# Kernel optimization log

Measured on AMD Instinct MI355X. Metric: run time of the kernel, lower is better.

The kernel has to match this reference:

```python
import jax, jax.numpy as jnp
import numpy as np

HEADS = 20
HEAD_DIM = 64  # 1280 / 20
IP_SCALE = 1.0


def _split_heads(x, B):
    # [B, S, H*D] -> [B, H, S, D]
    return x.reshape(B, -1, HEADS, HEAD_DIM).transpose(0, 2, 1, 3)


def _merge_heads(x, B):
    # [B, H, S, D] -> [B, S, H*D]
    return x.transpose(0, 2, 1, 3).reshape(B, -1, HEADS * HEAD_DIM)


def _sdpa(q, k, v):
    # q:[B,H,Sq,D] k,v:[B,H,Sk,D]
    scale = 1.0 / jnp.sqrt(jnp.asarray(HEAD_DIM, q.dtype))
    scores = jnp.einsum('bhqd,bhkd->bhqk', q, k) * scale
    probs = jax.nn.softmax(scores, axis=-1)
    return jnp.einsum('bhqk,bhkd->bhqd', probs, v)


def setup_inputs() -> dict:
    key = jax.random.key(0)
    ks = jax.random.split(key, 10)
    B, S, D = 8, 4096, 1280
    Ctx, Cdim = 77, 2048
    Adim = 768
    inp = {
        'hidden_states': jax.random.normal(ks[0], (B, S, D), jnp.float32),
        'encoder_hidden_states': jax.random.normal(ks[1], (B, Ctx, Cdim), jnp.float32),
        'adapter_embeds': jax.random.normal(ks[2], (B, 1, Adim), jnp.float32),
        'Wq': jax.random.normal(ks[3], (D, D), jnp.float32) * 0.02,
        'Wk': jax.random.normal(ks[4], (Cdim, D), jnp.float32) * 0.02,
        'Wv': jax.random.normal(ks[5], (Cdim, D), jnp.float32) * 0.02,
        'Wk_adapter': jax.random.normal(ks[6], (Adim, D), jnp.float32) * 0.02,
        'Wv_adapter': jax.random.normal(ks[7], (Adim, D), jnp.float32) * 0.02,
        'Wo': jax.random.normal(ks[8], (D, D), jnp.float32) * 0.02,
        'bo': jnp.zeros((D,), jnp.float32),
    }
    return inp


def reference(hidden_states, encoder_hidden_states, adapter_embeds,
              Wq, Wk, Wv, Wk_adapter, Wv_adapter, Wo, bo):
    B = hidden_states.shape[0]

    # base cross-attention projections
    q = _split_heads(hidden_states @ Wq, B)                 # [B,H,S,D]
    k = _split_heads(encoder_hidden_states @ Wk, B)         # [B,H,77,D]
    v = _split_heads(encoder_hidden_states @ Wv, B)
    out = _merge_heads(_sdpa(q, k, v), B)                   # [B,S,H*D]

    # IP-adapter branch: single-token K/V, shares the same query
    k_ip = _split_heads(adapter_embeds @ Wk_adapter, B)     # [B,H,1,D]
    v_ip = _split_heads(adapter_embeds @ Wv_adapter, B)
    out_ip = _merge_heads(_sdpa(q, k_ip, v_ip), B)

    merged = out + IP_SCALE * out_ip
    return merged @ Wo + bo
```

## Files before the change

### kernel.cpp

```cpp
#include <hip/hip_runtime.h>
#include <hip/hip_bf16.h>
#include <cstdint>
#include <cstddef>

typedef __hip_bfloat16 bf16_t;
typedef __attribute__((ext_vector_type(8))) __bf16 bf16x8;
typedef __attribute__((ext_vector_type(4))) float f32x4;

__device__ __forceinline__ void gld_lds16(const void* g, void* l) {
    __builtin_amdgcn_global_load_lds(
        (const __attribute__((address_space(1))) void*)(g),
        (__attribute__((address_space(3))) void*)(l), 16, 0, 0);
}

__global__ void k_cast(const float* __restrict__ in, bf16_t* __restrict__ out, long n) {
    long i = ((long)blockIdx.x * blockDim.x + threadIdx.x) * 4;
    if (i >= n) return;
    float4 v = *(const float4*)(in + i);
    out[i + 0] = __float2bfloat16(v.x);
    out[i + 1] = __float2bfloat16(v.y);
    out[i + 2] = __float2bfloat16(v.z);
    out[i + 3] = __float2bfloat16(v.w);
}

__global__ void k_cast_pad(const float* __restrict__ in, bf16_t* __restrict__ out,
                           int rows_in, int rows_out, int cols) {
    long i = ((long)blockIdx.x * blockDim.x + threadIdx.x) * 4;
    long n = (long)rows_out * cols;
    if (i >= n) return;
    int r = (int)(i / cols);
    if (r < rows_in) {
        float4 v = *(const float4*)(in + i);
        out[i + 0] = __float2bfloat16(v.x);
        out[i + 1] = __float2bfloat16(v.y);
        out[i + 2] = __float2bfloat16(v.z);
        out[i + 3] = __float2bfloat16(v.w);
    } else {
        bf16_t z = __float2bfloat16(0.f);
        out[i + 0] = z; out[i + 1] = z; out[i + 2] = z; out[i + 3] = z;
    }
}

__global__ void k_transpose_cast2(const float* __restrict__ in0, bf16_t* __restrict__ out0,
                                  const float* __restrict__ in1, bf16_t* __restrict__ out1,
                                  int R, int C) {
    __shared__ float tile[32][33];
    const float* in = blockIdx.z ? in1 : in0;
    bf16_t* out = blockIdx.z ? out1 : out0;
    int bx = blockIdx.x * 32;
    int by = blockIdx.y * 32;
    int tx = threadIdx.x & 31, ty = threadIdx.x >> 5;
    #pragma unroll
    for (int j = 0; j < 32; j += 8)
        tile[ty + j][tx] = in[(size_t)(by + ty + j) * C + bx + tx];
    __syncthreads();
    #pragma unroll
    for (int j = 0; j < 32; j += 8)
        out[(size_t)(bx + ty + j) * R + by + tx] = __float2bfloat16(tile[tx][ty + j]);
}

__global__ void k_adapter(const float* __restrict__ ae, const float* __restrict__ Wva,
                          float* __restrict__ vip) {
    int g = blockIdx.x * 256 + threadIdx.x;
    int b = g / 1280, n = g % 1280;
    const float* a = ae + b * 768;
    float acc = 0.f;
    for (int k = 0; k < 768; ++k) acc += a[k] * Wva[(size_t)k * 1280 + n];
    vip[g] = acc;
}

template <bool OUT_BF16, bool ADD_BIAS, bool SWZ>
__global__ __launch_bounds__(256, 2) void k_gemm_bt(
    const bf16_t* __restrict__ A, const bf16_t* __restrict__ Bt,
    void* __restrict__ Cv, const float* __restrict__ bias, int M, int N, int K,
    int snt, int mtx) {
    __shared__ __align__(16) bf16_t As[128 * 32];
    __shared__ __align__(16) bf16_t Bs[128 * 32];
    const int tid = threadIdx.x;
    int m0, n0;
    if constexpr (SWZ) {
        int id = blockIdx.x;
        int xcd = id & 7, j = id >> 3;
        m0 = (xcd * mtx + j / snt) * 128;
        n0 = (j % snt) * 128;
    } else {
        m0 = blockIdx.y * 128;
        n0 = blockIdx.x * 128;
    }
    const int wave = tid >> 6, lane = tid & 63;
    const int wm = (wave >> 1) * 64, wn = (wave & 1) * 64;
    const int quad = lane >> 4, l16 = lane & 15;

    f32x4 acc[4][4] = {};

    const int c0 = tid, c1 = tid + 256;
    const int r0 = c0 >> 2, o0 = (c0 & 3) * 8;
    const int r1 = c1 >> 2, o1 = (c1 & 3) * 8;
    const bf16_t* a0 = A + (size_t)(m0 + r0) * K + o0;
    const bf16_t* a1 = A + (size_t)(m0 + r1) * K + o1;
    const bf16_t* b0 = Bt + (size_t)(n0 + r0) * K + o0;
    const bf16_t* b1 = Bt + (size_t)(n0 + r1) * K + o1;

    for (int k0 = 0; k0 < K; k0 += 32) {
        __syncthreads();
        gld_lds16(a0 + k0, As + c0 * 8);
        gld_lds16(a1 + k0, As + c1 * 8);
        gld_lds16(b0 + k0, Bs + c0 * 8);
        gld_lds16(b1 + k0, Bs + c1 * 8);
        __syncthreads();
        bf16x8 af[4], bfv[4];
        #pragma unroll
        for (int t = 0; t < 4; ++t) {
            af[t]  = *(const bf16x8*)(As + (wm + t * 16 + l16) * 32 + quad * 8);
            bfv[t] = *(const bf16x8*)(Bs + (wn + t * 16 + l16) * 32 + quad * 8);
        }
        #pragma unroll
        for (int mt = 0; mt < 4; ++mt)
            #pragma unroll
            for (int nt = 0; nt < 4; ++nt)
                acc[mt][nt] = __builtin_amdgcn_mfma_f32_16x16x32_bf16(af[mt], bfv[nt], acc[mt][nt], 0, 0, 0);
    }

    if constexpr (OUT_BF16) {
        bf16_t* C = (bf16_t*)Cv;
        #pragma unroll
        for (int mt = 0; mt < 4; ++mt)
            #pragma unroll
            for (int rg = 0; rg < 4; ++rg) {
                int row = m0 + wm + mt * 16 + quad * 4 + rg;
                #pragma unroll
                for (int nt = 0; nt < 4; ++nt) {
                    int col = n0 + wn + nt * 16 + l16;
                    C[(size_t)row * N + col] = __float2bfloat16(acc[mt][nt][rg]);
                }
            }
    } else {
        float* C = (float*)Cv;
        float bv[4];
        #pragma unroll
        for (int nt = 0; nt < 4; ++nt)
            bv[nt] = ADD_BIAS ? bias[n0 + wn + nt * 16 + l16] : 0.f;
        #pragma unroll
        for (int mt = 0; mt < 4; ++mt)
            #pragma unroll
            for (int rg = 0; rg < 4; ++rg) {
                int row = m0 + wm + mt * 16 + quad * 4 + rg;
                #pragma unroll
                for (int nt = 0; nt < 4; ++nt) {
                    int col = n0 + wn + nt * 16 + l16;
                    C[(size_t)row * N + col] = acc[mt][nt][rg] + bv[nt];
                }
            }
    }
}

template <bool OUT_BF16, bool ADD_BIAS, int KC>
__global__ __launch_bounds__(512, 2) void k_gemm256(
    const bf16_t* __restrict__ A, const bf16_t* __restrict__ Bt,
    void* __restrict__ Cv, const float* __restrict__ bias,
    int N, int snt, int mtx) {
    __shared__ __align__(16) bf16_t As[2][256 * 64];
    __shared__ __align__(16) bf16_t Bs[2][256 * 64];
    const int tid = threadIdx.x;
    const int id = blockIdx.x;
    const int xcd = id & 7, jb = id >> 3;
    const int m0 = (xcd * mtx + jb / snt) * 256;
    const int n0 = (jb % snt) * 256;
    const int wave = tid >> 6, lane = tid & 63;
    const int wm = wave >> 2, wn = wave & 3;
    const int quad = lane >> 4, l16 = lane & 15;

    const int lr0 = tid >> 3;
    const int cst = ((tid & 7) * 8) ^ ((lr0 & 7) * 8);
    const bf16_t* pA0 = A + (size_t)(m0 + lr0) * KC + cst;
    const bf16_t* pA1 = pA0 + (size_t)128 * KC;
    const bf16_t* pB0 = Bt + (size_t)(n0 + ((lr0 >> 5) << 6) + (lr0 & 31)) * KC + cst;
    const bf16_t* pB1 = pB0 + (size_t)128 * KC;
    const int eA0 = tid * 8, eA1 = 4096 + tid * 8;

    const int xorc = (l16 & 7) * 8;
    const int c0x = (quad * 8) ^ xorc;
    const int c1x = (32 + quad * 8) ^ xorc;
    const int arow = (wm * 64 + l16) * 64;
    const int brow = (wn * 32 + l16) * 64;

    f32x4 acc[8][4] = {};
    bf16x8 afA[4][2], afB[4][2], bf0[2][2], bf1[2][2];

#define SA0_(WB, T) do { size_t ko_ = (size_t)(T) * 64; \
    gld_lds16(pA0 + ko_, &As[WB][eA0]); gld_lds16(pA1 + ko_, &As[WB][eA1]); } while (0)
#define SA1_(WB, T) do { size_t ko_ = (size_t)(T) * 64 + (size_t)64 * KC; \
    gld_lds16(pA0 + ko_, &As[WB][8192 + eA0]); gld_lds16(pA1 + ko_, &As[WB][8192 + eA1]); } while (0)
#define SB0_(WB, T) do { size_t ko_ = (size_t)(T) * 64; \
    gld_lds16(pB0 + ko_, &Bs[WB][eA0]); gld_lds16(pB1 + ko_, &Bs[WB][eA1]); } while (0)
#define SB1_(WB, T) do { size_t ko_ = (size_t)(T) * 64 + (size_t)32 * KC; \
    gld_lds16(pB0 + ko_, &Bs[WB][8192 + eA0]); gld_lds16(pB1 + ko_, &Bs[WB][8192 + eA1]); } while (0)
#define RD_AFA(RB_) do { _Pragma("unroll") for (int mt = 0; mt < 4; ++mt) { \
    const bf16_t* p_ = &As[RB_][arow + mt * 1024]; \
    afA[mt][0] = *(const bf16x8*)(p_ + c0x); afA[mt][1] = *(const bf16x8*)(p_ + c1x); } } while (0)
#define RD_AFB(RB_) do { _Pragma("unroll") for (int mt = 0; mt < 4; ++mt) { \
    const bf16_t* p_ = &As[RB_][8192 + arow + mt * 1024]; \
    afB[mt][0] = *(const bf16x8*)(p_ + c0x); afB[mt][1] = *(const bf16x8*)(p_ + c1x); } } while (0)
#define RD_BF0(RB_) do { _Pragma("unroll") for (int nt = 0; nt < 2; ++nt) { \
    const bf16_t* p_ = &Bs[RB_][brow + nt * 1024]; \
    bf0[nt][0] = *(const bf16x8*)(p_ + c0x); bf0[nt][1] = *(const bf16x8*)(p_ + c1x); } } while (0)
#define RD_BF1(RB_) do { _Pragma("unroll") for (int nt = 0; nt < 2; ++nt) { \
    const bf16_t* p_ = &Bs[RB_][8192 + brow + nt * 1024]; \
    bf1[nt][0] = *(const bf16x8*)(p_ + c0x); bf1[nt][1] = *(const bf16x8*)(p_ + c1x); } } while (0)
#define MMA_(AF, BF, MB, NB) do { _Pragma("unroll") \
    for (int mt = 0; mt < 4; ++mt) _Pragma("unroll") \
    for (int nt = 0; nt < 2; ++nt) _Pragma("unroll") \
    for (int ks = 0; ks < 2; ++ks) \
      acc[(MB) + mt][(NB) + nt] = __builtin_amdgcn_mfma_f32_16x16x32_bf16( \
          AF[mt][ks], BF[nt][ks], acc[(MB) + mt][(NB) + nt], 0, 0, 0); } while (0)
#define BAR_ asm volatile("s_barrier" ::: "memory")
#define VM_(n) asm volatile("s_waitcnt vmcnt(" #n ")" ::: "memory")
#define LG_(n) do { asm volatile("s_waitcnt lgkmcnt(" #n ")" ::: "memory"); \
    __builtin_amdgcn_sched_barrier(0); } while (0)
#define P1_ __builtin_amdgcn_s_setprio(1)
#define P0_ __builtin_amdgcn_s_setprio(0)

#define TILE_(T, RB) do { \
    RD_BF1(RB); SA1_((RB) ^ 1, (T) + 1); VM_(8); BAR_; \
    LG_(4); P1_; MMA_(afA, bf0, 0, 0); P0_; BAR_; \
    RD_AFB(RB); SA0_(RB, (T) + 2); VM_(8); BAR_; \
    LG_(8); P1_; MMA_(afA, bf1, 0, 2); P0_; BAR_; \
    RD_AFA((RB) ^ 1); SB0_(RB, (T) + 2); VM_(8); BAR_; \
    LG_(8); P1_; MMA_(afB, bf0, 4, 0); P0_; BAR_; \
    RD_BF0((RB) ^ 1); SB1_(RB, (T) + 2); VM_(8); BAR_; \
    P1_; MMA_(afB, bf1, 4, 2); P0_; BAR_; \
  } while (0)

    const int NT = KC >> 6;

    SA0_(0, 0); SB0_(0, 0); SB1_(0, 0); SA1_(0, 0);
    SA0_(1, 1); SB0_(1, 1); SB1_(1, 1);
    VM_(8);
    BAR_;
    RD_AFA(0); RD_BF0(0);

    #pragma unroll 1
    for (int t = 0; t < NT - 2; t += 2) {
        TILE_(t, 0);
        TILE_(t + 1, 1);
    }

    RD_BF1(0); SA1_(1, NT - 1); VM_(8); BAR_;
    LG_(4); P1_; MMA_(afA, bf0, 0, 0); P0_; BAR_;
    RD_AFB(0); VM_(6); BAR_;
    LG_(8); P1_; MMA_(afA, bf1, 0, 2); P0_; BAR_;
    RD_AFA(1); VM_(4); BAR_;
    LG_(8); P1_; MMA_(afB, bf0, 4, 0); P0_; BAR_;
    RD_BF0(1); VM_(2); BAR_;
    P1_; MMA_(afB, bf1, 4, 2); P0_; BAR_;
    RD_BF1(1); VM_(0); BAR_;
    RD_AFB(1);
    LG_(12); P1_; MMA_(afA, bf0, 0, 0); P0_;
    LG_(8);  P1_; MMA_(afA, bf1, 0, 2); P0_;
    LG_(0);  P1_; MMA_(afB, bf0, 4, 0); P0_;
    P1_; MMA_(afB, bf1, 4, 2); P0_;

#undef SA0_
#undef SA1_
#undef SB0_
#undef SB1_
#undef RD_AFA
#undef RD_AFB
#undef RD_BF0
#undef RD_BF1
#undef MMA_
#undef BAR_
#undef VM_
#undef LG_
#undef P1_
#undef P0_
#undef TILE_

    if constexpr (OUT_BF16) {
        bf16_t* C = (bf16_t*)Cv;
        __syncthreads();
        bf16_t* eb = wm ? (bf16_t*)Bs : (bf16_t*)As;
        #pragma unroll
        for (int mt = 0; mt < 8; ++mt)
            #pragma unroll
            for (int rg = 0; rg < 4; ++rg) {
                int rr = (mt >> 2) * 64 + (mt & 3) * 16 + quad * 4 + rg;
                #pragma unroll
                for (int nt = 0; nt < 4; ++nt)
                    eb[rr * 256 + wn * 64 + nt * 16 + l16] = __float2bfloat16(acc[mt][nt][rg]);
            }
        __syncthreads();
        #pragma unroll
        for (int pass = 0; pass < 16; ++pass) {
            const bf16_t* sb = (pass < 8) ? (const bf16_t*)As : (const bf16_t*)Bs;
            int r = pass * 16 + (tid >> 5);
            int cc = (tid & 31) * 8;
            *(int4*)(&C[(size_t)(m0 + r) * N + n0 + cc]) =
                *(const int4*)(sb + (r & 127) * 256 + cc);
        }
    } else {
        float* C = (float*)Cv;
        float bv[4];
        #pragma unroll
        for (int nt = 0; nt < 4; ++nt)
            bv[nt] = ADD_BIAS ? bias[n0 + wn * 64 + nt * 16 + l16] : 0.f;
        #pragma unroll
        for (int mt = 0; mt < 8; ++mt)
            #pragma unroll
            for (int rg = 0; rg < 4; ++rg) {
                int row = m0 + wm * 128 + (mt >> 2) * 64 + (mt & 3) * 16 + quad * 4 + rg;
                #pragma unroll
                for (int nt = 0; nt < 4; ++nt) {
                    int col = n0 + wn * 64 + nt * 16 + l16;
                    C[(size_t)row * N + col] = acc[mt][nt][rg] + bv[nt];
                }
            }
    }
}

__global__ __launch_bounds__(256, 2) void k_attn(
    const bf16_t* __restrict__ Q, const bf16_t* __restrict__ KV,
    const float* __restrict__ vip, bf16_t* __restrict__ Mrg) {
    __shared__ __align__(16) bf16_t Qs[128 * 64];
    __shared__ __align__(16) bf16_t Ks[96 * 64];
    __shared__ __align__(16) bf16_t Vt[64 * 96];
    __shared__ __align__(16) bf16_t Ps[128 * 96];
    const int tid = threadIdx.x;
    const int qb = blockIdx.x, h = blockIdx.y, b = blockIdx.z;
    const int wave = tid >> 6, lane = tid & 63;
    const int quad = lane >> 4, l16 = lane & 15;

    const bf16_t* Qg = Q + ((size_t)(b * 4096 + qb * 128)) * 1280 + h * 64;
    #pragma unroll
    for (int j = 0; j < 4; ++j) {
        int c = tid + j * 256;
        int r = c >> 3, o = (c & 7) * 8;
        gld_lds16(Qg + (size_t)r * 1280 + o, Qs + c * 8);
    }
    bf16_t z = __float2bfloat16(0.f);
    for (int i = 77 * 64 + tid; i < 96 * 64; i += 256) Ks[i] = z;
    for (int i = tid; i < 64 * 19; i += 256) {
        int d = i / 19, kk = 77 + i % 19;
        Vt[d * 96 + kk] = z;
    }
    for (int c = tid; c < 616; c += 256) {
        int r = c >> 3, o = (c & 7) * 8;
        size_t gi = ((size_t)(b * 77 + r)) * 2560 + h * 64 + o;
        int4 kv = *(const int4*)(KV + gi);
        *(int4*)(Ks + r * 64 + o) = kv;
        int4 vv = *(const int4*)(KV + gi + 1280);
        const bf16_t* ve = (const bf16_t*)&vv;
        #pragma unroll
        for (int j = 0; j < 8; ++j) Vt[(o + j) * 96 + r] = ve[j];
    }
    __syncthreads();

    f32x4 sacc[2][6] = {};
    #pragma unroll
    for (int ks = 0; ks < 2; ++ks) {
        bf16x8 aq[2], bk[6];
        #pragma unroll
        for (int mt = 0; mt < 2; ++mt)
            aq[mt] = *(const bf16x8*)(Qs + (wave * 32 + mt * 16 + l16) * 64 + ks * 32 + quad * 8);
        #pragma unroll
        for (int nt = 0; nt < 6; ++nt)
            bk[nt] = *(const bf16x8*)(Ks + (nt * 16 + l16) * 64 + ks * 32 + quad * 8);
        #pragma unroll
        for (int mt = 0; mt < 2; ++mt)
            #pragma unroll
            for (int nt = 0; nt < 6; ++nt)
                sacc[mt][nt] = __builtin_amdgcn_mfma_f32_16x16x32_bf16(aq[mt], bk[nt], sacc[mt][nt], 0, 0, 0);
    }
    #pragma unroll
    for (int mt = 0; mt < 2; ++mt)
        #pragma unroll
        for (int nt = 0; nt < 6; ++nt)
            #pragma unroll
            for (int rg = 0; rg < 4; ++rg) {
                int row = wave * 32 + mt * 16 + quad * 4 + rg;
                int col = nt * 16 + l16;
                Ps[row * 96 + col] = __float2bfloat16(sacc[mt][nt][rg] * 0.125f);
            }
    __syncthreads();

    {
        int row = tid >> 1, half = tid & 1;
        int cbeg = half ? 39 : 0, cend = half ? 77 : 39;
        bf16_t* prow = Ps + row * 96;
        float mx = -1e30f;
        for (int c = cbeg; c < cend; ++c) mx = fmaxf(mx, __bfloat162float(prow[c]));
        mx = fmaxf(mx, __shfl_xor(mx, 1));
        float sm = 0.f;
        for (int c = cbeg; c < cend; ++c) sm += __expf(__bfloat162float(prow[c]) - mx);
        sm += __shfl_xor(sm, 1);
        float inv = 1.f / sm;
        for (int c = cbeg; c < cend; ++c)
            prow[c] = __float2bfloat16(__expf(__bfloat162float(prow[c]) - mx) * inv);
    }
    __syncthreads();

    f32x4 oacc[2][4] = {};
    #pragma unroll
    for (int ks = 0; ks < 3; ++ks) {
        bf16x8 ap[2], bv[4];
        #pragma unroll
        for (int mt = 0; mt < 2; ++mt)
            ap[mt] = *(const bf16x8*)(Ps + (wave * 32 + mt * 16 + l16) * 96 + ks * 32 + quad * 8);
        #pragma unroll
        for (int nt = 0; nt < 4; ++nt)
            bv[nt] = *(const bf16x8*)(Vt + (nt * 16 + l16) * 96 + ks * 32 + quad * 8);
        #pragma unroll
        for (int mt = 0; mt < 2; ++mt)
            #pragma unroll
            for (int nt = 0; nt < 4; ++nt)
                oacc[mt][nt] = __builtin_amdgcn_mfma_f32_16x16x32_bf16(ap[mt], bv[nt], oacc[mt][nt], 0, 0, 0);
    }
    __syncthreads();
    #pragma unroll
    for (int nt = 0; nt < 4; ++nt) {
        int col = nt * 16 + l16;
        float add = vip[b * 1280 + h * 64 + col];
        #pragma unroll
        for (int mt = 0; mt < 2; ++mt)
            #pragma unroll
            for (int rg = 0; rg < 4; ++rg) {
                int row = wave * 32 + mt * 16 + quad * 4 + rg;
                Ps[row * 64 + col] = __float2bfloat16(oacc[mt][nt][rg] + add);
            }
    }
    __syncthreads();
    #pragma unroll
    for (int pass = 0; pass < 4; ++pass) {
        int r = pass * 32 + (tid >> 3);
        int cc = (tid & 7) * 8;
        *(int4*)(Mrg + ((size_t)(b * 4096 + qb * 128 + r)) * 1280 + h * 64 + cc) =
            *(const int4*)(Ps + r * 64 + cc);
    }
}

extern "C" void kernel_launch(void* const* d_in, const int* in_sizes, int n_in,
                              void* d_out, int out_size, void* d_ws, size_t ws_size,
                              hipStream_t stream) {
    (void)in_sizes; (void)n_in; (void)out_size; (void)ws_size;
    const float* hs  = (const float*)d_in[0];
    const float* enc = (const float*)d_in[1];
    const float* ae  = (const float*)d_in[2];
    const float* Wq  = (const float*)d_in[3];
    const float* Wk  = (const float*)d_in[4];
    const float* Wv  = (const float*)d_in[5];
    const float* Wva = (const float*)d_in[7];
    const float* Wo  = (const float*)d_in[8];
    const float* bo  = (const float*)d_in[9];
    float* out = (float*)d_out;

    char* ws = (char*)d_ws;
    size_t off = 0;
    auto alloc = [&](size_t bytes) -> void* {
        void* p = ws + off;
        off += (bytes + 255) & ~(size_t)255;
        return p;
    };
    bf16_t* Xb   = (bf16_t*)alloc((size_t)32768 * 1280 * 2);
    bf16_t* Qb   = (bf16_t*)alloc((size_t)32768 * 1280 * 2);
    bf16_t* Mrg  = (bf16_t*)alloc((size_t)32768 * 1280 * 2);
    bf16_t* Eb   = (bf16_t*)alloc((size_t)640 * 2048 * 2);
    bf16_t* WqT  = (bf16_t*)alloc((size_t)1280 * 1280 * 2);
    bf16_t* WkvT = (bf16_t*)alloc((size_t)2560 * 2048 * 2);
    bf16_t* WoT  = (bf16_t*)alloc((size_t)1280 * 1280 * 2);
    bf16_t* KVc  = (bf16_t*)alloc((size_t)640 * 2560 * 2);
    float*  vip  = (float*)alloc((size_t)8 * 1280 * 4);

    k_cast<<<40960, 256, 0, stream>>>(hs, Xb, (long)32768 * 1280);
    k_cast_pad<<<1280, 256, 0, stream>>>(enc, Eb, 616, 640, 2048);
    k_transpose_cast2<<<dim3(40, 40, 2), 256, 0, stream>>>(Wq, WqT, Wo, WoT, 1280, 1280);
    k_transpose_cast2<<<dim3(40, 64, 2), 256, 0, stream>>>(Wk, WkvT, Wv, WkvT + (size_t)1280 * 2048, 2048, 1280);
    k_adapter<<<40, 256, 0, stream>>>(ae, Wva, vip);

    k_gemm256<true, false, 1280><<<640, 512, 0, stream>>>(Xb, WqT, Qb, nullptr, 1280, 5, 16);
    k_gemm_bt<true, false, false><<<dim3(20, 5), 256, 0, stream>>>(Eb, WkvT, KVc, nullptr, 640, 2560, 2048, 0, 0);

    k_attn<<<dim3(32, 20, 8), 256, 0, stream>>>(Qb, KVc, vip, Mrg);

    k_gemm256<false, true, 1280><<<640, 512, 0, stream>>>(Mrg, WoT, out, bo, 1280, 5, 16);
}
```

Measured before the change: 830.8 us.

## Merge prolog kernels, fold KV GEMM into Q GEMM launch, register-resident softmax

Fuses the hidden-state and encoder casts into one launch and the four weight transposes into another. It folds the small encoder K/V projection into the large Q-projection GEMM grid as extra blocks, with K now a runtime value. The GEMM main loop's waitcnt/barrier schedule changes, and attention softmax now runs on MFMA accumulators in registers with shuffles instead of a shared-memory pass. The LDS strides for P and V are padded to avoid bank conflicts. This cuts launch count and a shared-memory round trip, but runtime K may cost some loop codegen quality and the retuned wait counts risk subtle hazards.

```diff
diff --git a/kernel.cpp b/kernel.cpp
--- a/kernel.cpp
+++ b/kernel.cpp
@@ -13,40 +13,43 @@
         (__attribute__((address_space(3))) void*)(l), 16, 0, 0);
 }
 
-__global__ void k_cast(const float* __restrict__ in, bf16_t* __restrict__ out, long n) {
-    long i = ((long)blockIdx.x * blockDim.x + threadIdx.x) * 4;
-    if (i >= n) return;
-    float4 v = *(const float4*)(in + i);
-    out[i + 0] = __float2bfloat16(v.x);
-    out[i + 1] = __float2bfloat16(v.y);
-    out[i + 2] = __float2bfloat16(v.z);
-    out[i + 3] = __float2bfloat16(v.w);
-}
-
-__global__ void k_cast_pad(const float* __restrict__ in, bf16_t* __restrict__ out,
-                           int rows_in, int rows_out, int cols) {
-    long i = ((long)blockIdx.x * blockDim.x + threadIdx.x) * 4;
-    long n = (long)rows_out * cols;
-    if (i >= n) return;
-    int r = (int)(i / cols);
-    if (r < rows_in) {
-        float4 v = *(const float4*)(in + i);
-        out[i + 0] = __float2bfloat16(v.x);
-        out[i + 1] = __float2bfloat16(v.y);
-        out[i + 2] = __float2bfloat16(v.z);
-        out[i + 3] = __float2bfloat16(v.w);
+__global__ void k_prolog(const float* __restrict__ hs, bf16_t* __restrict__ Xb,
+                         const float* __restrict__ enc, bf16_t* __restrict__ Eb) {
+    if (blockIdx.x < 40960) {
+        long i = ((long)blockIdx.x * 256 + threadIdx.x) * 4;
+        float4 v = *(const float4*)(hs + i);
+        Xb[i + 0] = __float2bfloat16(v.x);
+        Xb[i + 1] = __float2bfloat16(v.y);
+        Xb[i + 2] = __float2bfloat16(v.z);
+        Xb[i + 3] = __float2bfloat16(v.w);
     } else {
-        bf16_t z = __float2bfloat16(0.f);
-        out[i + 0] = z; out[i + 1] = z; out[i + 2] = z; out[i + 3] = z;
-    }
-}
-
-__global__ void k_transpose_cast2(const float* __restrict__ in0, bf16_t* __restrict__ out0,
-                                  const float* __restrict__ in1, bf16_t* __restrict__ out1,
-                                  int R, int C) {
+        long i = ((long)(blockIdx.x - 40960) * 256 + threadIdx.x) * 4;
+        int r = (int)(i / 2048);
+        if (r < 616) {
+            float4 v = *(const float4*)(enc + i);
+            Eb[i + 0] = __float2bfloat16(v.x);
+            Eb[i + 1] = __float2bfloat16(v.y);
+            Eb[i + 2] = __float2bfloat16(v.z);
+            Eb[i + 3] = __float2bfloat16(v.w);
+        } else {
+            bf16_t z = __float2bfloat16(0.f);
+            Eb[i + 0] = z; Eb[i + 1] = z; Eb[i + 2] = z; Eb[i + 3] = z;
+        }
+    }
+}
+
+__global__ void k_transpose_cast4(const float* __restrict__ Wq, bf16_t* __restrict__ WqT,
+                                  const float* __restrict__ Wo, bf16_t* __restrict__ WoT,
+                                  const float* __restrict__ Wk, const float* __restrict__ Wv,
+                                  bf16_t* __restrict__ WkvT) {
     __shared__ float tile[32][33];
-    const float* in = blockIdx.z ? in1 : in0;
-    bf16_t* out = blockIdx.z ? out1 : out0;
+    int z = blockIdx.z;
+    if (z < 2 && blockIdx.y >= 40) return;
+    const float* in; bf16_t* out; int R, C;
+    if (z == 0)      { in = Wq; out = WqT; R = 1280; C = 1280; }
+    else if (z == 1) { in = Wo; out = WoT; R = 1280; C = 1280; }
+    else if (z == 2) { in = Wk; out = WkvT; R = 2048; C = 1280; }
+    else             { in = Wv; out = WkvT + (size_t)1280 * 2048; R = 2048; C = 1280; }
     int bx = blockIdx.x * 32;
     int by = blockIdx.y * 32;
     int tx = threadIdx.x & 31, ty = threadIdx.x >> 5;
@@ -69,113 +72,40 @@
     vip[g] = acc;
 }
 
-template <bool OUT_BF16, bool ADD_BIAS, bool SWZ>
-__global__ __launch_bounds__(256, 2) void k_gemm_bt(
-    const bf16_t* __restrict__ A, const bf16_t* __restrict__ Bt,
-    void* __restrict__ Cv, const float* __restrict__ bias, int M, int N, int K,
-    int snt, int mtx) {
-    __shared__ __align__(16) bf16_t As[128 * 32];
-    __shared__ __align__(16) bf16_t Bs[128 * 32];
-    const int tid = threadIdx.x;
-    int m0, n0;
-    if constexpr (SWZ) {
-        int id = blockIdx.x;
-        int xcd = id & 7, j = id >> 3;
-        m0 = (xcd * mtx + j / snt) * 128;
-        n0 = (j % snt) * 128;
-    } else {
-        m0 = blockIdx.y * 128;
-        n0 = blockIdx.x * 128;
-    }
-    const int wave = tid >> 6, lane = tid & 63;
-    const int wm = (wave >> 1) * 64, wn = (wave & 1) * 64;
-    const int quad = lane >> 4, l16 = lane & 15;
-
-    f32x4 acc[4][4] = {};
-
-    const int c0 = tid, c1 = tid + 256;
-    const int r0 = c0 >> 2, o0 = (c0 & 3) * 8;
-    const int r1 = c1 >> 2, o1 = (c1 & 3) * 8;
-    const bf16_t* a0 = A + (size_t)(m0 + r0) * K + o0;
-    const bf16_t* a1 = A + (size_t)(m0 + r1) * K + o1;
-    const bf16_t* b0 = Bt + (size_t)(n0 + r0) * K + o0;
-    const bf16_t* b1 = Bt + (size_t)(n0 + r1) * K + o1;
-
-    for (int k0 = 0; k0 < K; k0 += 32) {
-        __syncthreads();
-        gld_lds16(a0 + k0, As + c0 * 8);
-        gld_lds16(a1 + k0, As + c1 * 8);
-        gld_lds16(b0 + k0, Bs + c0 * 8);
-        gld_lds16(b1 + k0, Bs + c1 * 8);
-        __syncthreads();
-        bf16x8 af[4], bfv[4];
-        #pragma unroll
-        for (int t = 0; t < 4; ++t) {
-            af[t]  = *(const bf16x8*)(As + (wm + t * 16 + l16) * 32 + quad * 8);
-            bfv[t] = *(const bf16x8*)(Bs + (wn + t * 16 + l16) * 32 + quad * 8);
-        }
-        #pragma unroll
-        for (int mt = 0; mt < 4; ++mt)
-            #pragma unroll
-            for (int nt = 0; nt < 4; ++nt)
-                acc[mt][nt] = __builtin_amdgcn_mfma_f32_16x16x32_bf16(af[mt], bfv[nt], acc[mt][nt], 0, 0, 0);
-    }
-
-    if constexpr (OUT_BF16) {
-        bf16_t* C = (bf16_t*)Cv;
-        #pragma unroll
-        for (int mt = 0; mt < 4; ++mt)
-            #pragma unroll
-            for (int rg = 0; rg < 4; ++rg) {
-                int row = m0 + wm + mt * 16 + quad * 4 + rg;
-                #pragma unroll
-                for (int nt = 0; nt < 4; ++nt) {
-                    int col = n0 + wn + nt * 16 + l16;
-                    C[(size_t)row * N + col] = __float2bfloat16(acc[mt][nt][rg]);
-                }
-            }
-    } else {
-        float* C = (float*)Cv;
-        float bv[4];
-        #pragma unroll
-        for (int nt = 0; nt < 4; ++nt)
-            bv[nt] = ADD_BIAS ? bias[n0 + wn + nt * 16 + l16] : 0.f;
-        #pragma unroll
-        for (int mt = 0; mt < 4; ++mt)
-            #pragma unroll
-            for (int rg = 0; rg < 4; ++rg) {
-                int row = m0 + wm + mt * 16 + quad * 4 + rg;
-                #pragma unroll
-                for (int nt = 0; nt < 4; ++nt) {
-                    int col = n0 + wn + nt * 16 + l16;
-                    C[(size_t)row * N + col] = acc[mt][nt][rg] + bv[nt];
-                }
-            }
-    }
-}
-
-template <bool OUT_BF16, bool ADD_BIAS, int KC>
+template <bool OUT_BF16, bool ADD_BIAS>
 __global__ __launch_bounds__(512, 2) void k_gemm256(
     const bf16_t* __restrict__ A, const bf16_t* __restrict__ Bt,
     void* __restrict__ Cv, const float* __restrict__ bias,
-    int N, int snt, int mtx) {
+    int N, int K, int snt, int mtx, int nq,
+    const bf16_t* __restrict__ A2, const bf16_t* __restrict__ Bt2,
+    bf16_t* __restrict__ C2, int N2, int K2, int snt2) {
     __shared__ __align__(16) bf16_t As[2][256 * 64];
     __shared__ __align__(16) bf16_t Bs[2][256 * 64];
     const int tid = threadIdx.x;
     const int id = blockIdx.x;
-    const int xcd = id & 7, jb = id >> 3;
-    const int m0 = (xcd * mtx + jb / snt) * 256;
-    const int n0 = (jb % snt) * 256;
+    const bf16_t* Ain; const bf16_t* Btin; void* Cout;
+    int Nn, Kd, m0, n0;
+    if (id < nq) {
+        int xcd = id & 7, j = id >> 3;
+        m0 = (xcd * mtx + j / snt) * 256;
+        n0 = (j % snt) * 256;
+        Ain = A; Btin = Bt; Cout = Cv; Nn = N; Kd = K;
+    } else {
+        int j = id - nq;
+        m0 = (j / snt2) * 256;
+        n0 = (j % snt2) * 256;
+        Ain = A2; Btin = Bt2; Cout = (void*)C2; Nn = N2; Kd = K2;
+    }
     const int wave = tid >> 6, lane = tid & 63;
     const int wm = wave >> 2, wn = wave & 3;
     const int quad = lane >> 4, l16 = lane & 15;
 
     const int lr0 = tid >> 3;
     const int cst = ((tid & 7) * 8) ^ ((lr0 & 7) * 8);
-    const bf16_t* pA0 = A + (size_t)(m0 + lr0) * KC + cst;
-    const bf16_t* pA1 = pA0 + (size_t)128 * KC;
-    const bf16_t* pB0 = Bt + (size_t)(n0 + ((lr0 >> 5) << 6) + (lr0 & 31)) * KC + cst;
-    const bf16_t* pB1 = pB0 + (size_t)128 * KC;
+    const bf16_t* pA0 = Ain + (size_t)(m0 + lr0) * Kd + cst;
+    const bf16_t* pA1 = pA0 + (size_t)128 * Kd;
+    const bf16_t* pB0 = Btin + (size_t)(n0 + ((lr0 >> 5) << 6) + (lr0 & 31)) * Kd + cst;
+    const bf16_t* pB1 = pB0 + (size_t)128 * Kd;
     const int eA0 = tid * 8, eA1 = 4096 + tid * 8;
 
     const int xorc = (l16 & 7) * 8;
@@ -189,11 +119,11 @@
 
 #define SA0_(WB, T) do { size_t ko_ = (size_t)(T) * 64; \
     gld_lds16(pA0 + ko_, &As[WB][eA0]); gld_lds16(pA1 + ko_, &As[WB][eA1]); } while (0)
-#define SA1_(WB, T) do { size_t ko_ = (size_t)(T) * 64 + (size_t)64 * KC; \
+#define SA1_(WB, T) do { size_t ko_ = (size_t)(T) * 64 + (size_t)64 * Kd; \
     gld_lds16(pA0 + ko_, &As[WB][8192 + eA0]); gld_lds16(pA1 + ko_, &As[WB][8192 + eA1]); } while (0)
 #define SB0_(WB, T) do { size_t ko_ = (size_t)(T) * 64; \
     gld_lds16(pB0 + ko_, &Bs[WB][eA0]); gld_lds16(pB1 + ko_, &Bs[WB][eA1]); } while (0)
-#define SB1_(WB, T) do { size_t ko_ = (size_t)(T) * 64 + (size_t)32 * KC; \
+#define SB1_(WB, T) do { size_t ko_ = (size_t)(T) * 64 + (size_t)32 * Kd; \
     gld_lds16(pB0 + ko_, &Bs[WB][8192 + eA0]); gld_lds16(pB1 + ko_, &Bs[WB][8192 + eA1]); } while (0)
 #define RD_AFA(RB_) do { _Pragma("unroll") for (int mt = 0; mt < 4; ++mt) { \
     const bf16_t* p_ = &As[RB_][arow + mt * 1024]; \
@@ -220,38 +150,46 @@
 #define P1_ __builtin_amdgcn_s_setprio(1)
 #define P0_ __builtin_amdgcn_s_setprio(0)
 
-#define TILE_(T, RB) do { \
-    RD_BF1(RB); SA1_((RB) ^ 1, (T) + 1); VM_(8); BAR_; \
-    LG_(4); P1_; MMA_(afA, bf0, 0, 0); P0_; BAR_; \
-    RD_AFB(RB); SA0_(RB, (T) + 2); VM_(8); BAR_; \
-    LG_(8); P1_; MMA_(afA, bf1, 0, 2); P0_; BAR_; \
-    RD_AFA((RB) ^ 1); SB0_(RB, (T) + 2); VM_(8); BAR_; \
-    LG_(8); P1_; MMA_(afB, bf0, 4, 0); P0_; BAR_; \
-    RD_BF0((RB) ^ 1); SB1_(RB, (T) + 2); VM_(8); BAR_; \
+#define TILEFULL(T, RB) do { \
+    RD_BF1(RB); SA1_((RB) ^ 1, (T) + 1); \
+    asm volatile("s_waitcnt lgkmcnt(8)" ::: "memory"); \
+    BAR_; LG_(0); \
+    P1_; MMA_(afA, bf0, 0, 0); P0_; BAR_; \
+    RD_AFB(RB); SA0_(RB, (T) + 2); \
+    BAR_; LG_(0); \
+    P1_; MMA_(afA, bf1, 0, 2); P0_; BAR_; \
+    RD_AFA((RB) ^ 1); SB0_(RB, (T) + 2); \
+    BAR_; LG_(0); \
+    P1_; MMA_(afB, bf0, 4, 0); P0_; BAR_; \
+    RD_BF0((RB) ^ 1); SB1_(RB, (T) + 2); \
+    VM_(6); \
+    BAR_; LG_(0); \
     P1_; MMA_(afB, bf1, 4, 2); P0_; BAR_; \
   } while (0)
 
-    const int NT = KC >> 6;
+    const int NT = Kd >> 6;
 
     SA0_(0, 0); SB0_(0, 0); SB1_(0, 0); SA1_(0, 0);
     SA0_(1, 1); SB0_(1, 1); SB1_(1, 1);
-    VM_(8);
+    VM_(6);
     BAR_;
     RD_AFA(0); RD_BF0(0);
 
     #pragma unroll 1
     for (int t = 0; t < NT - 2; t += 2) {
-        TILE_(t, 0);
-        TILE_(t + 1, 1);
-    }
-
-    RD_BF1(0); SA1_(1, NT - 1); VM_(8); BAR_;
-    LG_(4); P1_; MMA_(afA, bf0, 0, 0); P0_; BAR_;
-    RD_AFB(0); VM_(6); BAR_;
-    LG_(8); P1_; MMA_(afA, bf1, 0, 2); P0_; BAR_;
-    RD_AFA(1); VM_(4); BAR_;
-    LG_(8); P1_; MMA_(afB, bf0, 4, 0); P0_; BAR_;
-    RD_BF0(1); VM_(2); BAR_;
+        TILEFULL(t, 0);
+        TILEFULL(t + 1, 1);
+    }
+
+    RD_BF1(0); SA1_(1, NT - 1);
+    asm volatile("s_waitcnt lgkmcnt(8)" ::: "memory");
+    BAR_; LG_(0);
+    P1_; MMA_(afA, bf0, 0, 0); P0_; BAR_;
+    RD_AFB(0); VM_(6); BAR_; LG_(0);
+    P1_; MMA_(afA, bf1, 0, 2); P0_; BAR_;
+    RD_AFA(1); VM_(4); BAR_; LG_(0);
+    P1_; MMA_(afB, bf0, 4, 0); P0_; BAR_;
+    RD_BF0(1); VM_(2); BAR_; LG_(0);
     P1_; MMA_(afB, bf1, 4, 2); P0_; BAR_;
     RD_BF1(1); VM_(0); BAR_;
     RD_AFB(1);
@@ -274,10 +212,10 @@
 #undef LG_
 #undef P1_
 #undef P0_
-#undef TILE_
+#undef TILEFULL
 
     if constexpr (OUT_BF16) {
-        bf16_t* C = (bf16_t*)Cv;
+        bf16_t* C = (bf16_t*)Cout;
         __syncthreads();
         bf16_t* eb = wm ? (bf16_t*)Bs : (bf16_t*)As;
         #pragma unroll
@@ -295,11 +233,11 @@
             const bf16_t* sb = (pass < 8) ? (const bf16_t*)As : (const bf16_t*)Bs;
             int r = pass * 16 + (tid >> 5);
             int cc = (tid & 31) * 8;
-            *(int4*)(&C[(size_t)(m0 + r) * N + n0 + cc]) =
+            *(int4*)(&C[(size_t)(m0 + r) * Nn + n0 + cc]) =
                 *(const int4*)(sb + (r & 127) * 256 + cc);
         }
     } else {
-        float* C = (float*)Cv;
+        float* C = (float*)Cout;
         float bv[4];
         #pragma unroll
         for (int nt = 0; nt < 4; ++nt)
@@ -312,7 +250,7 @@
                 #pragma unroll
                 for (int nt = 0; nt < 4; ++nt) {
                     int col = n0 + wn * 64 + nt * 16 + l16;
-                    C[(size_t)row * N + col] = acc[mt][nt][rg] + bv[nt];
+                    C[(size_t)row * Nn + col] = acc[mt][nt][rg] + bv[nt];
                 }
             }
     }
@@ -321,10 +259,11 @@
 __global__ __launch_bounds__(256, 2) void k_attn(
     const bf16_t* __restrict__ Q, const bf16_t* __restrict__ KV,
     const float* __restrict__ vip, bf16_t* __restrict__ Mrg) {
+    constexpr int PST = 104, VST = 104;
     __shared__ __align__(16) bf16_t Qs[128 * 64];
     __shared__ __align__(16) bf16_t Ks[96 * 64];
-    __shared__ __align__(16) bf16_t Vt[64 * 96];
-    __shared__ __align__(16) bf16_t Ps[128 * 96];
+    __shared__ __align__(16) bf16_t Vt[64 * VST];
+    __shared__ __align__(16) bf16_t Ps[128 * PST];
     const int tid = threadIdx.x;
     const int qb = blockIdx.x, h = blockIdx.y, b = blockIdx.z;
     const int wave = tid >> 6, lane = tid & 63;
@@ -341,7 +280,7 @@
     for (int i = 77 * 64 + tid; i < 96 * 64; i += 256) Ks[i] = z;
     for (int i = tid; i < 64 * 19; i += 256) {
         int d = i / 19, kk = 77 + i % 19;
-        Vt[d * 96 + kk] = z;
+        Vt[d * VST + kk] = z;
     }
     for (int c = tid; c < 616; c += 256) {
         int r = c >> 3, o = (c & 7) * 8;
@@ -351,7 +290,7 @@
         int4 vv = *(const int4*)(KV + gi + 1280);
         const bf16_t* ve = (const bf16_t*)&vv;
         #pragma unroll
-        for (int j = 0; j < 8; ++j) Vt[(o + j) * 96 + r] = ve[j];
+        for (int j = 0; j < 8; ++j) Vt[(o + j) * VST + r] = ve[j];
     }
     __syncthreads();
 
@@ -371,31 +310,40 @@
             for (int nt = 0; nt < 6; ++nt)
                 sacc[mt][nt] = __builtin_amdgcn_mfma_f32_16x16x32_bf16(aq[mt], bk[nt], sacc[mt][nt], 0, 0, 0);
     }
-    #pragma unroll
-    for (int mt = 0; mt < 2; ++mt)
-        #pragma unroll
-        for (int nt = 0; nt < 6; ++nt)
-            #pragma unroll
-            for (int rg = 0; rg < 4; ++rg) {
-                int row = wave * 32 + mt * 16 + quad * 4 + rg;
+
+    #pragma unroll
+    for (int mt = 0; mt < 2; ++mt) {
+        #pragma unroll
+        for (int rg = 0; rg < 4; ++rg) {
+            float v[6];
+            float mx = -1e30f;
+            #pragma unroll
+            for (int nt = 0; nt < 6; ++nt) {
                 int col = nt * 16 + l16;
-                Ps[row * 96 + col] = __float2bfloat16(sacc[mt][nt][rg] * 0.125f);
+                v[nt] = sacc[mt][nt][rg] * 0.125f;
+                if (col < 77) mx = fmaxf(mx, v[nt]);
             }
-    __syncthreads();
-
-    {
-        int row = tid >> 1, half = tid & 1;
-        int cbeg = half ? 39 : 0, cend = half ? 77 : 39;
-        bf16_t* prow = Ps + row * 96;
-        float mx = -1e30f;
-        for (int c = cbeg; c < cend; ++c) mx = fmaxf(mx, __bfloat162float(prow[c]));
-        mx = fmaxf(mx, __shfl_xor(mx, 1));
-        float sm = 0.f;
-        for (int c = cbeg; c < cend; ++c) sm += __expf(__bfloat162float(prow[c]) - mx);
-        sm += __shfl_xor(sm, 1);
-        float inv = 1.f / sm;
-        for (int c = cbeg; c < cend; ++c)
-            prow[c] = __float2bfloat16(__expf(__bfloat162float(prow[c]) - mx) * inv);
+            mx = fmaxf(mx, __shfl_xor(mx, 1));
+            mx = fmaxf(mx, __shfl_xor(mx, 2));
+            mx = fmaxf(mx, __shfl_xor(mx, 4));
+            mx = fmaxf(mx, __shfl_xor(mx, 8));
+            float sm = 0.f;
+            #pragma unroll
+            for (int nt = 0; nt < 6; ++nt) {
+                int col = nt * 16 + l16;
+                v[nt] = (col < 77) ? __expf(v[nt] - mx) : 0.f;
+                sm += v[nt];
+            }
+            sm += __shfl_xor(sm, 1);
+            sm += __shfl_xor(sm, 2);
+            sm += __shfl_xor(sm, 4);
+            sm += __shfl_xor(sm, 8);
+            float inv = 1.f / sm;
+            int row = wave * 32 + mt * 16 + quad * 4 + rg;
+            #pragma unroll
+            for (int nt = 0; nt < 6; ++nt)
+                Ps[row * PST + nt * 16 + l16] = __float2bfloat16(v[nt] * inv);
+        }
     }
     __syncthreads();
 
@@ -405,10 +353,10 @@
         bf16x8 ap[2], bv[4];
         #pragma unroll
         for (int mt = 0; mt < 2; ++mt)
-            ap[mt] = *(const bf16x8*)(Ps + (wave * 32 + mt * 16 + l16) * 96 + ks * 32 + quad * 8);
+            ap[mt] = *(const bf16x8*)(Ps + (wave * 32 + mt * 16 + l16) * PST + ks * 32 + quad * 8);
         #pragma unroll
         for (int nt = 0; nt < 4; ++nt)
-            bv[nt] = *(const bf16x8*)(Vt + (nt * 16 + l16) * 96 + ks * 32 + quad * 8);
+            bv[nt] = *(const bf16x8*)(Vt + (nt * 16 + l16) * VST + ks * 32 + quad * 8);
         #pragma unroll
         for (int mt = 0; mt < 2; ++mt)
             #pragma unroll
@@ -463,23 +411,24 @@
     bf16_t* Xb   = (bf16_t*)alloc((size_t)32768 * 1280 * 2);
     bf16_t* Qb   = (bf16_t*)alloc((size_t)32768 * 1280 * 2);
     bf16_t* Mrg  = (bf16_t*)alloc((size_t)32768 * 1280 * 2);
-    bf16_t* Eb   = (bf16_t*)alloc((size_t)640 * 2048 * 2);
+    bf16_t* Eb   = (bf16_t*)alloc((size_t)768 * 2048 * 2);
     bf16_t* WqT  = (bf16_t*)alloc((size_t)1280 * 1280 * 2);
     bf16_t* WkvT = (bf16_t*)alloc((size_t)2560 * 2048 * 2);
     bf16_t* WoT  = (bf16_t*)alloc((size_t)1280 * 1280 * 2);
-    bf16_t* KVc  = (bf16_t*)alloc((size_t)640 * 2560 * 2);
+    bf16_t* KVc  = (bf16_t*)alloc((size_t)768 * 2560 * 2);
     float*  vip  = (float*)alloc((size_t)8 * 1280 * 4);
 
-    k_cast<<<40960, 256, 0, stream>>>(hs, Xb, (long)32768 * 1280);
-    k_cast_pad<<<1280, 256, 0, stream>>>(enc, Eb, 616, 640, 2048);
-    k_transpose_cast2<<<dim3(40, 40, 2), 256, 0, stream>>>(Wq, WqT, Wo, WoT, 1280, 1280);
-    k_transpose_cast2<<<dim3(40, 64, 2), 256, 0, stream>>>(Wk, WkvT, Wv, WkvT + (size_t)1280 * 2048, 2048, 1280);
+    k_prolog<<<40960 + 1536, 256, 0, stream>>>(hs, Xb, enc, Eb);
+    k_transpose_cast4<<<dim3(40, 64, 4), 256, 0, stream>>>(Wq, WqT, Wo, WoT, Wk, Wv, WkvT);
     k_adapter<<<40, 256, 0, stream>>>(ae, Wva, vip);
 
-    k_gemm256<true, false, 1280><<<640, 512, 0, stream>>>(Xb, WqT, Qb, nullptr, 1280, 5, 16);
-    k_gemm_bt<true, false, false><<<dim3(20, 5), 256, 0, stream>>>(Eb, WkvT, KVc, nullptr, 640, 2560, 2048, 0, 0);
+    k_gemm256<true, false><<<670, 512, 0, stream>>>(
+        Xb, WqT, Qb, nullptr, 1280, 1280, 5, 16, 640,
+        Eb, WkvT, KVc, 2560, 2048, 10);
 
     k_attn<<<dim3(32, 20, 8), 256, 0, stream>>>(Qb, KVc, vip, Mrg);
 
-    k_gemm256<false, true, 1280><<<640, 512, 0, stream>>>(Mrg, WoT, out, bo, 1280, 5, 16);
-}
+    k_gemm256<false, true><<<640, 512, 0, stream>>>(
+        Mrg, WoT, out, bo, 1280, 1280, 5, 16, 640,
+        nullptr, nullptr, nullptr, 0, 0, 1);
+}
```

Measured after the change: 1.014 ms. +22.0%, slower.
